# Performance work log

Hardware: AMD Instinct MI355X
Metric: run time of the kernel (lower is better)

## Reference

```python
import jax, jax.numpy as jnp
import numpy as np
from jax import lax

B, T, N, D, M, K, H = 16, 96, 256, 128, 1196, 8, 4
HD = D // H  # head dim = 32
TAU_TIME = 2.0


def setup_inputs() -> dict:
    key = jax.random.key(0)
    ks = jax.random.split(key, 12)
    w = lambda k, shp: jax.random.normal(k, shp, jnp.float32) * 0.05
    return {
        "x_scalar": jax.random.normal(ks[0], (B, T, N), jnp.float32),
        "season_q": jax.random.randint(ks[1], (B,), 0, 4),
        "year_q": 2010.0 + 10.0 * jax.random.uniform(ks[2], (B,), jnp.float32),
        "dw_w": w(ks[3], (N, 1, 12)),          # depthwise Conv1d weight (out=N, in/groups=1, k=12)
        "dw_b": jnp.zeros((N,), jnp.float32),
        "pw_w": w(ks[4], (N * D, N)),          # pointwise Conv1d weight (out=N*D, in=N), k=1 squeezed
        "pw_b": jnp.zeros((N * D,), jnp.float32),
        "ln_g": jnp.ones((D,), jnp.float32),
        "ln_b": jnp.zeros((D,), jnp.float32),
        "memory_bank": jax.random.normal(ks[5], (M, N, D), jnp.float32),
        "memory_seasons": jax.random.randint(ks[6], (M,), 0, 4),
        "memory_years": 2010.0 + 10.0 * jax.random.uniform(ks[7], (M,), jnp.float32),
        "in_proj_w": w(ks[8], (3 * D, D)),     # MHA packed q/k/v projection
        "in_proj_b": jnp.zeros((3 * D,), jnp.float32),
        "out_proj_w": w(ks[9], (D, D)),
        "out_proj_b": jnp.zeros((D,), jnp.float32),
        "proj_w": w(ks[10], (D, D)),
        "proj_b": jnp.zeros((D,), jnp.float32),
    }


def _layernorm(x, g, b, eps=1e-5):
    mu = jnp.mean(x, axis=-1, keepdims=True)
    var = jnp.mean((x - mu) ** 2, axis=-1, keepdims=True)
    return (x - mu) * lax.rsqrt(var + eps) * g + b


def _l2norm(x, eps=1e-12):
    n = jnp.sqrt(jnp.sum(x * x, axis=-1, keepdims=True))
    return x / jnp.maximum(n, eps)


def _forward(x_scalar, season_q, year_q, dw_w, dw_b, pw_w, pw_b, ln_g, ln_b,
             memory_bank, memory_seasons, memory_years,
             in_proj_w, in_proj_b, out_proj_w, out_proj_b, proj_w, proj_b):
    b, t, n = x_scalar.shape
    d = ln_g.shape[0]
    m = memory_bank.shape[0]

    # --- TemporalEncoder ---
    x = jnp.transpose(x_scalar, (0, 2, 1))  # (b, n, t): permute(0,2,3,1).reshape with d_input=1
    x = lax.conv_general_dilated(
        x, dw_w, window_strides=(1,), padding=[(6, 6)],
        dimension_numbers=("NCH", "OIH", "NCH"), feature_group_count=n)
    x = jax.nn.gelu(x + dw_b[:, None], approximate=False)      # (b, n, t+1)
    x = jnp.einsum("bct,oc->bot", x, pw_w) + pw_b[:, None]     # pointwise 1x1 conv -> (b, n*d, t+1)
    x = jax.nn.gelu(x, approximate=False)
    x = jnp.mean(x, axis=-1).reshape(b, n, d)                  # adaptive avg pool to 1
    q = _layernorm(x, ln_g, ln_b)                              # (b, n, d)

    # --- retrieve ---
    qf = _l2norm(q.reshape(b, n * d))
    memf = _l2norm(memory_bank.reshape(m, n * d))
    sim = qf @ memf.T                                          # (b, m)
    smask = (season_q[:, None] == memory_seasons[None, :]).astype(sim.dtype)
    sim = sim * smask + (1.0 - smask) * (-10000.0)
    dy = jnp.abs(year_q[:, None] - memory_years[None, :])
    diversity = 1.0 - jnp.exp(-dy / max(TAU_TIME, 1e-4))
    sim = sim * (0.5 + 0.5 * diversity)
    _, idx = lax.top_k(sim, K)                                 # (b, K)
    retrieved = memory_bank[idx]                               # (b, K, n, d)

    # --- cross attention: query (b*n, 1, d) vs kv (b*n, K, d) ---
    Wq, Wk, Wv = in_proj_w[:d], in_proj_w[d:2 * d], in_proj_w[2 * d:]
    bq, bk, bv = in_proj_b[:d], in_proj_b[d:2 * d], in_proj_b[2 * d:]
    kv = jnp.transpose(retrieved, (0, 2, 1, 3))                # (b, n, K, d)
    qp = (jnp.einsum("bnd,ed->bne", q, Wq) + bq).reshape(b, n, H, HD)
    kp = (jnp.einsum("bnkd,ed->bnke", kv, Wk) + bk).reshape(b, n, K, H, HD)
    vp = (jnp.einsum("bnkd,ed->bnke", kv, Wv) + bv).reshape(b, n, K, H, HD)
    scores = jnp.einsum("bnhe,bnkhe->bnhk", qp, kp) / np.sqrt(HD)
    attn = jax.nn.softmax(scores, axis=-1)
    ctx = jnp.einsum("bnhk,bnkhe->bnhe", attn, vp).reshape(b, n, d)
    out = jnp.einsum("bnd,ed->bne", ctx, out_proj_w) + out_proj_b
    out = jnp.einsum("bnd,ed->bne", out, proj_w) + proj_b
    return out, q


def reference(x_scalar, season_q, year_q, dw_w, dw_b, pw_w, pw_b, ln_g, ln_b,
              memory_bank, memory_seasons, memory_years,
              in_proj_w, in_proj_b, out_proj_w, out_proj_b, proj_w, proj_b):
    return _forward(x_scalar, season_q, year_q, dw_w, dw_b, pw_w, pw_b, ln_g, ln_b,
                    memory_bank, memory_seasons, memory_years,
                    in_proj_w, in_proj_b, out_proj_w, out_proj_b, proj_w, proj_b)
```

## Files before the change

kernel.cpp:

```cpp
#include <hip/hip_runtime.h>

typedef _Float16 f16x8 __attribute__((ext_vector_type(8)));
typedef _Float16 f16x4 __attribute__((ext_vector_type(4)));
typedef float    f32x4 __attribute__((ext_vector_type(4)));

__device__ __forceinline__ float gelu_f(float x) {
    float z  = 0.70710678118654752440f * x;
    float az = fabsf(z);
    float t  = 1.0f / fmaf(0.3275911f, az, 1.0f);
    float e  = __expf(-az * az);
    float p  = t * fmaf(t, fmaf(t, fmaf(t, fmaf(t, 1.061405429f, -1.453152027f),
                                        1.421413741f), -0.284496736f), 0.254829592f);
    float er = fmaf(-p, e, 1.0f);
    float s  = (z < 0.0f) ? -er : er;
    return 0.5f * x * (1.0f + s);
}

__device__ __forceinline__ void gload16(const void* g, void* l) {
    __builtin_amdgcn_global_load_lds(
        (const __attribute__((address_space(1))) unsigned int*)g,
        (__attribute__((address_space(3))) unsigned int*)l, 16, 0, 0);
}

__global__ void conv_kernel(const float* __restrict__ xs, const float* __restrict__ dww,
                            const float* __restrict__ dwb, _Float16* __restrict__ Gt)
{
    int b = blockIdx.x, t = blockIdx.y, n = threadIdx.x;
    float g = 0.f;
    if (t < 97) {
        float y = 0.f;
        #pragma unroll
        for (int j = 0; j < 12; ++j) {
            int tt = t + j - 6;
            if (tt >= 0 && tt < 96)
                y += dww[n*12 + j] * xs[((size_t)b*96 + tt)*256 + n];
        }
        g = gelu_f(y + dwb[n]);
    }
    Gt[((size_t)b*128 + t)*256 + n] = (_Float16)g;
}

__global__ void cvt_pw_kernel(const float* __restrict__ src, _Float16* __restrict__ dst,
                              const float* __restrict__ ipw, const float* __restrict__ opw,
                              const float* __restrict__ pjw, const float* __restrict__ opb,
                              const float* __restrict__ pjb, _Float16* __restrict__ wAll,
                              float* __restrict__ zp, _Float16* __restrict__ Wcf,
                              float* __restrict__ bc)
{
    int bid = blockIdx.x, tid = threadIdx.x;
    if (bid < 8192) {
        size_t i = ((size_t)bid*256 + tid) * 4;
        float4 v = *(const float4*)&src[i];
        f16x4 o; o[0] = (_Float16)v.x; o[1] = (_Float16)v.y; o[2] = (_Float16)v.z; o[3] = (_Float16)v.w;
        *(f16x4*)&dst[i] = o;
    } else if (bid < 8512) {
        int i = (bid - 8192)*256 + tid;
        float v = (i < 49152) ? ipw[i] : (i < 65536 ? opw[i - 49152] : pjw[i - 65536]);
        wAll[i] = (_Float16)v;
    } else if (bid < 8532) {
        int i = (bid - 8512)*256 + tid;
        if (i < 5087) {
            float4 z = {0.f, 0.f, 0.f, 0.f};
            *(float4*)&zp[i*4] = z;
        }
    } else {
        int e = (bid - 8532)*2 + (tid >> 7);
        int c = tid & 127;
        float acc = 0.f;
        for (int d = 0; d < 128; ++d)
            acc = fmaf(pjw[e*128 + d], opw[d*128 + c], acc);
        Wcf[e*128 + c] = (_Float16)acc;
        if (c == 0) {
            float s = pjb[e];
            for (int d = 0; d < 128; ++d)
                s = fmaf(pjw[e*128 + d], opb[d], s);
            bc[e] = s;
        }
    }
}

__global__ __launch_bounds__(256) void pw_kernel(const _Float16* __restrict__ W,
                                                 const _Float16* __restrict__ Gt,
                                                 const float* __restrict__ pwb,
                                                 const float* __restrict__ lng,
                                                 const float* __restrict__ lnb,
                                                 float* __restrict__ qout,
                                                 _Float16* __restrict__ qh,
                                                 _Float16* __restrict__ qlo,
                                                 float* __restrict__ qss)
{
    __shared__ __align__(16) _Float16 As[2][128][32];
    __shared__ __align__(16) _Float16 Bs[2][128][32];

    int x = blockIdx.x;
    int xcd = x & 7, ii = x >> 3;
    int ob = xcd * 32 + (ii >> 4);
    int b  = ii & 15;
    const _Float16* Arow = W  + (size_t)ob * 128 * 256;
    const _Float16* Brow = Gt + (size_t)b  * 128 * 256;

    int tid = threadIdx.x, w = tid >> 6, l = tid & 63, lr = l & 15, lk = l >> 4;
    int wr = w >> 1, wc = w & 1;
    int rsw = (lr >> 1) & 3;

    f32x4 acc[4][4];
    #pragma unroll
    for (int i = 0; i < 4; ++i)
        #pragma unroll
        for (int j = 0; j < 4; ++j)
            acc[i][j] = f32x4{0.f, 0.f, 0.f, 0.f};

    auto stage = [&](int buf, int k0) {
        #pragma unroll
        for (int j = 0; j < 2; ++j) {
            int chunk = tid + j*256;
            int row = chunk >> 2;
            int co  = (chunk & 3) * 8;
            int cos = ((chunk & 3) ^ ((chunk >> 3) & 3)) * 8;
            gload16(&Arow[row*256 + k0 + cos], &As[buf][row][co]);
            gload16(&Brow[row*256 + k0 + cos], &Bs[buf][row][co]);
        }
    };

    stage(0, 0);
    __syncthreads();
    for (int ks = 0; ks < 8; ++ks) {
        int cur = ks & 1;
        if (ks < 7) stage(cur ^ 1, (ks + 1) * 32);
        f16x8 a[4], bb[4];
        #pragma unroll
        for (int i = 0; i < 4; ++i)
            a[i]  = *(const f16x8*)&As[cur][wr*64 + i*16 + lr][(lk ^ rsw)*8];
        #pragma unroll
        for (int j = 0; j < 4; ++j)
            if (wc == 0 || j < 3)
                bb[j] = *(const f16x8*)&Bs[cur][wc*64 + j*16 + lr][(lk ^ rsw)*8];
        #pragma unroll
        for (int i = 0; i < 4; ++i)
            #pragma unroll
            for (int j = 0; j < 4; ++j)
                if (wc == 0 || j < 3)
                    acc[i][j] = __builtin_amdgcn_mfma_f32_16x16x32_f16(bb[j], a[i], acc[i][j], 0, 0, 0);
        __syncthreads();
    }

    float (*red)[2] = reinterpret_cast<float(*)[2]>(&As[0][0][0]);
    #pragma unroll
    for (int i = 0; i < 4; ++i) {
        int og = ob*128 + wr*64 + i*16 + lr;
        float pbv = pwb[og];
        float s = 0.f;
        if (wc == 0) {
            #pragma unroll
            for (int j = 0; j < 4; ++j)
                #pragma unroll
                for (int r = 0; r < 4; ++r)
                    s += gelu_f(acc[i][j][r] + pbv);
        } else {
            #pragma unroll
            for (int j = 0; j < 2; ++j)
                #pragma unroll
                for (int r = 0; r < 4; ++r)
                    s += gelu_f(acc[i][j][r] + pbv);
            if (lk == 0) s += gelu_f(acc[i][2][0] + pbv);
        }
        s += __shfl_xor(s, 16, 64);
        s += __shfl_xor(s, 32, 64);
        if (lk == 0) red[wr*64 + i*16 + lr][wc] = s;
    }
    __syncthreads();

    if (w == 0) {
        float x0 = (red[l][0]      + red[l][1])      * (1.f/97.f);
        float x1 = (red[64 + l][0] + red[64 + l][1]) * (1.f/97.f);
        float sm = x0 + x1;
        #pragma unroll
        for (int m = 1; m < 64; m <<= 1) sm += __shfl_xor(sm, m, 64);
        float mu = sm * (1.f/128.f);
        float d0 = x0 - mu, d1 = x1 - mu;
        float vv = d0*d0 + d1*d1;
        #pragma unroll
        for (int m = 1; m < 64; m <<= 1) vv += __shfl_xor(vv, m, 64);
        float rs = 1.0f / sqrtf(vv * (1.f/128.f) + 1e-5f);
        float q0 = d0*rs*lng[l]      + lnb[l];
        float q1 = d1*rs*lng[64 + l] + lnb[64 + l];
        size_t bn = (size_t)b*256 + ob;
        qout[bn*128 + l]      = q0;
        qout[bn*128 + 64 + l] = q1;
        _Float16 h0 = (_Float16)q0, h1 = (_Float16)q1;
        qh[bn*128 + l]       = h0;
        qh[bn*128 + 64 + l]  = h1;
        qlo[bn*128 + l]      = (_Float16)(q0 - (float)h0);
        qlo[bn*128 + 64 + l] = (_Float16)(q1 - (float)h1);
        float ss = q0*q0 + q1*q1;
        #pragma unroll
        for (int m = 1; m < 64; m <<= 1) ss += __shfl_xor(ss, m, 64);
        if (l == 0) atomicAdd(&qss[b], ss);
    }
}

__global__ __launch_bounds__(256) void simgemm_kernel(const _Float16* __restrict__ qhi,
                                                      const _Float16* __restrict__ qlo,
                                                      const float* __restrict__ mem,
                                                      float* __restrict__ dotp,
                                                      float* __restrict__ mn2)
{
    __shared__ __align__(16) float Ms[2][16][256];
    __shared__ f32x4 redls[4][64];
    __shared__ float redn[4][16];

    int tid = threadIdx.x, w = tid >> 6, l = tid & 63, lr = l & 15, lk = l >> 4;
    int m0 = blockIdx.y * 16;
    int kwin = blockIdx.x * 1024;
    int rowm = m0 + lr;

    auto stage = [&](int buf, int sw) {
        #pragma unroll
        for (int j = 0; j < 4; ++j) {
            int r = w*4 + j;
            int rowg = m0 + r; if (rowg > 1195) rowg = 1195;
            const float* src = mem + (size_t)rowg*32768 + kwin + sw*256 + (l ^ (r & 7))*4;
            gload16(src, &Ms[buf][r][0]);
        }
    };

    f32x4 acc_a = {0.f,0.f,0.f,0.f}, acc_b = {0.f,0.f,0.f,0.f};
    float nacc = 0.f;

    stage(0, 0);
    __syncthreads();
    for (int sw = 0; sw < 4; ++sw) {
        int cur = sw & 1;
        if (sw < 3) stage(cur ^ 1, sw + 1);
        #pragma unroll
        for (int cc = 0; cc < 2; ++cc) {
            int kl = w*64 + cc*32;
            int s0 = (kl + lk*8) >> 2;
            float4 v0 = *(const float4*)&Ms[cur][lr][(s0       ^ (lr & 7))*4];
            float4 v1 = *(const float4*)&Ms[cur][lr][((s0 + 1) ^ (lr & 7))*4];
            int kg = kwin + sw*256 + kl + lk*8;
            f16x8 ah = *(const f16x8*)&qhi[(size_t)lr*32768 + kg];
            f16x8 al = *(const f16x8*)&qlo[(size_t)lr*32768 + kg];
            float e0 = v0.x, e1 = v0.y, e2 = v0.z, e3 = v0.w;
            float e4 = v1.x, e5 = v1.y, e6 = v1.z, e7 = v1.w;
            f16x8 bh;
            bh[0]=(_Float16)e0; bh[1]=(_Float16)e1; bh[2]=(_Float16)e2; bh[3]=(_Float16)e3;
            bh[4]=(_Float16)e4; bh[5]=(_Float16)e5; bh[6]=(_Float16)e6; bh[7]=(_Float16)e7;
            nacc = fmaf(e0,e0, fmaf(e1,e1, fmaf(e2,e2, fmaf(e3,e3, nacc))));
            nacc = fmaf(e4,e4, fmaf(e5,e5, fmaf(e6,e6, fmaf(e7,e7, nacc))));
            acc_a = __builtin_amdgcn_mfma_f32_16x16x32_f16(ah, bh, acc_a, 0, 0, 0);
            acc_b = __builtin_amdgcn_mfma_f32_16x16x32_f16(al, bh, acc_b, 0, 0, 0);
        }
        __syncthreads();
    }

    nacc += __shfl_xor(nacc, 16, 64);
    nacc += __shfl_xor(nacc, 32, 64);

    f32x4 tot = acc_a + acc_b;
    redls[w][l] = tot;
    if (lk == 0) redn[w][lr] = nacc;
    __syncthreads();
    if (w == 0) {
        tot = redls[0][l];
        tot += redls[1][l]; tot += redls[2][l]; tot += redls[3][l];
        if (rowm < 1196) {
            #pragma unroll
            for (int r = 0; r < 4; ++r)
                atomicAdd(&dotp[(lk*4 + r)*1196 + rowm], tot[r]);
            if (lk == 0)
                atomicAdd(&mn2[rowm], redn[0][lr] + redn[1][lr] + redn[2][lr] + redn[3][lr]);
        }
    }
}

__global__ void topk_kernel(const float* __restrict__ dotp, const float* __restrict__ mn2,
                            const float* __restrict__ qss, const int* __restrict__ seaq,
                            const float* __restrict__ yq, const int* __restrict__ seam,
                            const float* __restrict__ ym, int* __restrict__ idx)
{
    __shared__ float sc[1216];
    int b = blockIdx.x, lane = threadIdx.x;
    float qn = fmaxf(sqrtf(qss[b]), 1e-12f);
    int sq = seaq[b];
    float yqv = yq[b];
    for (int m = lane; m < 1216; m += 64) {
        float v = -3e38f;
        if (m < 1196) {
            float s = dotp[b*1196 + m] / (qn * fmaxf(sqrtf(mn2[m]), 1e-12f));
            if (seam[m] != sq) s = -10000.0f;
            float dy = fabsf(yqv - ym[m]);
            v = s * (1.0f - 0.5f * expf(-0.5f * dy));
        }
        sc[m] = v;
    }
    __syncthreads();
    for (int kk = 0; kk < 8; ++kk) {
        float bv = -3e38f; int bi = 0x7fffffff;
        for (int m = lane; m < 1216; m += 64) {
            float v = sc[m];
            if (v > bv) { bv = v; bi = m; }
        }
        #pragma unroll
        for (int mk = 1; mk < 64; mk <<= 1) {
            float ov = __shfl_xor(bv, mk, 64);
            int   oi = __shfl_xor(bi, mk, 64);
            if (ov > bv || (ov == bv && oi < bi)) { bv = ov; bi = oi; }
        }
        if (lane == 0) { idx[b*8 + kk] = bi; sc[bi] = -3e38f; }
        __syncthreads();
    }
}

__global__ __launch_bounds__(256) void qkv_kernel(const _Float16* __restrict__ qh,
                                                  const float* __restrict__ memb,
                                                  const int* __restrict__ idx,
                                                  const _Float16* __restrict__ wAll,
                                                  const float* __restrict__ ipb,
                                                  _Float16* __restrict__ qp,
                                                  _Float16* __restrict__ kp,
                                                  _Float16* __restrict__ vp)
{
    int bid = blockIdx.x;
    const _Float16* Wm; const float* bias; _Float16* Y; int blk; int kv;
    if (bid < 64)       { kv = 0; Wm = wAll;         bias = ipb;       Y = qp; blk = bid; }
    else if (bid < 576) { kv = 1; Wm = wAll + 16384; bias = ipb + 128; Y = kp; blk = bid - 64; }
    else                { kv = 1; Wm = wAll + 32768; bias = ipb + 256; Y = vp; blk = bid - 576; }

    int tid = threadIdx.x, w = tid >> 6, l = tid & 63, lr = l & 15, lk = l >> 4;
    int r0 = blk * 64 + w * 16;

    const float* Af = nullptr;
    const _Float16* Ah = nullptr;
    if (kv) {
        int bk = (blk * 64) >> 8;
        int row = idx[bk];
        Af = memb + (size_t)row*32768 + ((r0 & 255) + lr)*128 + lk*8;
    } else {
        Ah = qh + (size_t)(r0 + lr)*128 + lk*8;
    }

    f32x4 acc[8];
    #pragma unroll
    for (int j = 0; j < 8; ++j) acc[j] = f32x4{0.f, 0.f, 0.f, 0.f};
    #pragma unroll
    for (int k0 = 0; k0 < 128; k0 += 32) {
        f16x8 a;
        if (kv) {
            float4 v0 = *(const float4*)&Af[k0];
            float4 v1 = *(const float4*)&Af[k0 + 4];
            a[0]=(_Float16)v0.x; a[1]=(_Float16)v0.y; a[2]=(_Float16)v0.z; a[3]=(_Float16)v0.w;
            a[4]=(_Float16)v1.x; a[5]=(_Float16)v1.y; a[6]=(_Float16)v1.z; a[7]=(_Float16)v1.w;
        } else {
            a = *(const f16x8*)&Ah[k0];
        }
        #pragma unroll
        for (int j = 0; j < 8; ++j) {
            f16x8 bb = *(const f16x8*)&Wm[(j*16 + lr)*128 + k0 + lk*8];
            acc[j] = __builtin_amdgcn_mfma_f32_16x16x32_f16(a, bb, acc[j], 0, 0, 0);
        }
    }
    #pragma unroll
    for (int j = 0; j < 8; ++j) {
        #pragma unroll
        for (int r = 0; r < 4; ++r) {
            int row = r0 + lk*4 + r, col = j*16 + lr;
            Y[(size_t)row*128 + col] = (_Float16)(acc[j][r] + bias[col]);
        }
    }
}

__global__ void attn_kernel(const _Float16* __restrict__ qp, const _Float16* __restrict__ kp,
                            const _Float16* __restrict__ vp, const _Float16* __restrict__ Wc,
                            const float* __restrict__ bc, float* __restrict__ outp)
{
    __shared__ float ctxs[128];
    int bn = blockIdx.x;
    int b = bn >> 8, n = bn & 255;
    int tid = threadIdx.x;
    float qv = (float)qp[(size_t)bn*128 + tid];
    float sc[8];
    #pragma unroll
    for (int k = 0; k < 8; ++k) {
        float p = qv * (float)kp[(((size_t)(b*8 + k)*256 + n)*128) + tid];
        #pragma unroll
        for (int m = 1; m < 32; m <<= 1) p += __shfl_xor(p, m, 64);
        sc[k] = p * 0.17677669529663687f;
    }
    float mx = sc[0];
    #pragma unroll
    for (int k = 1; k < 8; ++k) mx = fmaxf(mx, sc[k]);
    float den = 0.f;
    #pragma unroll
    for (int k = 0; k < 8; ++k) { sc[k] = expf(sc[k] - mx); den += sc[k]; }
    float inv = 1.f / den;
    float c = 0.f;
    #pragma unroll
    for (int k = 0; k < 8; ++k)
        c += sc[k] * (float)vp[(((size_t)(b*8 + k)*256 + n)*128) + tid];
    ctxs[tid] = c * inv;
    __syncthreads();

    float s = bc[tid];
    const f16x8* wrow = (const f16x8*)&Wc[(size_t)tid*128];
    #pragma unroll
    for (int c0 = 0; c0 < 16; ++c0) {
        f16x8 wv = wrow[c0];
        #pragma unroll
        for (int u = 0; u < 8; ++u)
            s = fmaf(ctxs[c0*8 + u], (float)wv[u], s);
    }
    outp[(size_t)bn*128 + tid] = s;
}

extern "C" void kernel_launch(void* const* d_in, const int* in_sizes, int n_in,
                              void* d_out, int out_size, void* d_ws, size_t ws_size,
                              hipStream_t stream)
{
    const float* x_scalar = (const float*)d_in[0];
    const int*   season_q = (const int*)d_in[1];
    const float* year_q   = (const float*)d_in[2];
    const float* dw_w     = (const float*)d_in[3];
    const float* dw_b     = (const float*)d_in[4];
    const float* pw_w     = (const float*)d_in[5];
    const float* pw_b     = (const float*)d_in[6];
    const float* ln_g     = (const float*)d_in[7];
    const float* ln_b     = (const float*)d_in[8];
    const float* memb     = (const float*)d_in[9];
    const int*   mseas    = (const int*)d_in[10];
    const float* myear    = (const float*)d_in[11];
    const float* ipw      = (const float*)d_in[12];
    const float* ipb      = (const float*)d_in[13];
    const float* opw      = (const float*)d_in[14];
    const float* opb      = (const float*)d_in[15];
    const float* pjw      = (const float*)d_in[16];
    const float* pjb      = (const float*)d_in[17];

    char* wsb = (char*)d_ws;
    _Float16* Wf   = (_Float16*)(wsb + 0);
    _Float16* Gt   = (_Float16*)(wsb + 16777216);
    float*    qss  = (float*)   (wsb + 20971520);
    float*    dotp = (float*)   (wsb + 20971584);
    float*    mn2  = (float*)   (wsb + 21048128);
    int*      idxb = (int*)     (wsb + 21052928);
    _Float16* qp   = (_Float16*)(wsb + 29442048);
    _Float16* kp   = (_Float16*)(wsb + 30490624);
    _Float16* vp   = (_Float16*)(wsb + 38879232);
    _Float16* Wcf  = (_Float16*)(wsb + 48316416);
    float*    bc   = (float*)   (wsb + 48349184);
    _Float16* wAll = (_Float16*)(wsb + 49364992);
    _Float16* qlo  = (_Float16*)(wsb + 49528832);
    _Float16* qh   = (_Float16*)(wsb + 19922944);

    float* outp = (float*)d_out;
    float* qout = (float*)d_out + 524288;

    cvt_pw_kernel<<<8596, 256, 0, stream>>>(pw_w, Wf, ipw, opw, pjw, opb, pjb, wAll,
                                            (float*)(wsb + 20971520), Wcf, bc);
    conv_kernel<<<dim3(16, 128), 256, 0, stream>>>(x_scalar, dw_w, dw_b, Gt);

    pw_kernel<<<4096, 256, 0, stream>>>(Wf, Gt, pw_b, ln_g, ln_b, qout, qh, qlo, qss);

    simgemm_kernel<<<dim3(32, 75), 256, 0, stream>>>(qh, qlo, memb, dotp, mn2);
    topk_kernel<<<16, 64, 0, stream>>>(dotp, mn2, qss, season_q, year_q, mseas, myear, idxb);

    qkv_kernel<<<1088, 256, 0, stream>>>(qh, memb, idxb, wAll, ipb, qp, kp, vp);

    attn_kernel<<<4096, 128, 0, stream>>>(qp, kp, vp, Wcf, bc, outp);
}
```

Before: 203.6 us.

## Tile-transpose query halves for simgemm loads and fuse K/V projections

```diff
diff --git a/kernel.cpp b/kernel.cpp
--- a/kernel.cpp
+++ b/kernel.cpp
@@ -86,7 +86,8 @@
                                                  const float* __restrict__ lnb,
                                                  float* __restrict__ qout,
                                                  _Float16* __restrict__ qh,
-                                                 _Float16* __restrict__ qlo,
+                                                 _Float16* __restrict__ qhT,
+                                                 _Float16* __restrict__ qloT,
                                                  float* __restrict__ qss)
 {
     __shared__ __align__(16) _Float16 As[2][128][32];
@@ -190,8 +191,12 @@
         _Float16 h0 = (_Float16)q0, h1 = (_Float16)q1;
         qh[bn*128 + l]       = h0;
         qh[bn*128 + 64 + l]  = h1;
-        qlo[bn*128 + l]      = (_Float16)(q0 - (float)h0);
-        qlo[bn*128 + 64 + l] = (_Float16)(q1 - (float)h1);
+        int ch0 = ob*4 + (l >> 5);
+        int sub = b*32 + ((l >> 3) & 3)*8 + (l & 7);
+        qhT [ch0*512 + sub]       = h0;
+        qhT [(ch0 + 2)*512 + sub] = h1;
+        qloT[ch0*512 + sub]       = (_Float16)(q0 - (float)h0);
+        qloT[(ch0 + 2)*512 + sub] = (_Float16)(q1 - (float)h1);
         float ss = q0*q0 + q1*q1;
         #pragma unroll
         for (int m = 1; m < 64; m <<= 1) ss += __shfl_xor(ss, m, 64);
@@ -199,8 +204,8 @@
     }
 }
 
-__global__ __launch_bounds__(256) void simgemm_kernel(const _Float16* __restrict__ qhi,
-                                                      const _Float16* __restrict__ qlo,
+__global__ __launch_bounds__(256) void simgemm_kernel(const _Float16* __restrict__ qhT,
+                                                      const _Float16* __restrict__ qloT,
                                                       const float* __restrict__ mem,
                                                       float* __restrict__ dotp,
                                                       float* __restrict__ mn2)
@@ -238,9 +243,10 @@
             int s0 = (kl + lk*8) >> 2;
             float4 v0 = *(const float4*)&Ms[cur][lr][(s0       ^ (lr & 7))*4];
             float4 v1 = *(const float4*)&Ms[cur][lr][((s0 + 1) ^ (lr & 7))*4];
-            int kg = kwin + sw*256 + kl + lk*8;
-            f16x8 ah = *(const f16x8*)&qhi[(size_t)lr*32768 + kg];
-            f16x8 al = *(const f16x8*)&qlo[(size_t)lr*32768 + kg];
+            int chunk = (kwin + sw*256 + kl) >> 5;
+            int fo = lr*4 + lk;
+            f16x8 ah = ((const f16x8*)(qhT  + (size_t)chunk*512))[fo];
+            f16x8 al = ((const f16x8*)(qloT + (size_t)chunk*512))[fo];
             float e0 = v0.x, e1 = v0.y, e2 = v0.z, e3 = v0.w;
             float e4 = v1.x, e5 = v1.y, e6 = v1.z, e7 = v1.w;
             f16x8 bh;
@@ -322,50 +328,66 @@
                                                   _Float16* __restrict__ vp)
 {
     int bid = blockIdx.x;
-    const _Float16* Wm; const float* bias; _Float16* Y; int blk; int kv;
-    if (bid < 64)       { kv = 0; Wm = wAll;         bias = ipb;       Y = qp; blk = bid; }
-    else if (bid < 576) { kv = 1; Wm = wAll + 16384; bias = ipb + 128; Y = kp; blk = bid - 64; }
-    else                { kv = 1; Wm = wAll + 32768; bias = ipb + 256; Y = vp; blk = bid - 576; }
-
     int tid = threadIdx.x, w = tid >> 6, l = tid & 63, lr = l & 15, lk = l >> 4;
-    int r0 = blk * 64 + w * 16;
-
-    const float* Af = nullptr;
-    const _Float16* Ah = nullptr;
-    if (kv) {
+
+    if (bid < 64) {
+        int r0 = bid * 64 + w * 16;
+        const _Float16* Ah = qh + (size_t)(r0 + lr)*128 + lk*8;
+        f32x4 acc[8];
+        #pragma unroll
+        for (int j = 0; j < 8; ++j) acc[j] = f32x4{0.f, 0.f, 0.f, 0.f};
+        #pragma unroll
+        for (int k0 = 0; k0 < 128; k0 += 32) {
+            f16x8 a = *(const f16x8*)&Ah[k0];
+            #pragma unroll
+            for (int j = 0; j < 8; ++j) {
+                f16x8 bb = *(const f16x8*)&wAll[(j*16 + lr)*128 + k0 + lk*8];
+                acc[j] = __builtin_amdgcn_mfma_f32_16x16x32_f16(a, bb, acc[j], 0, 0, 0);
+            }
+        }
+        #pragma unroll
+        for (int j = 0; j < 8; ++j) {
+            #pragma unroll
+            for (int r = 0; r < 4; ++r) {
+                int row = r0 + lk*4 + r, col = j*16 + lr;
+                qp[(size_t)row*128 + col] = (_Float16)(acc[j][r] + ipb[col]);
+            }
+        }
+    } else {
+        int blk = bid - 64;
+        int r0 = blk * 64 + w * 16;
         int bk = (blk * 64) >> 8;
         int row = idx[bk];
-        Af = memb + (size_t)row*32768 + ((r0 & 255) + lr)*128 + lk*8;
-    } else {
-        Ah = qh + (size_t)(r0 + lr)*128 + lk*8;
-    }
-
-    f32x4 acc[8];
-    #pragma unroll
-    for (int j = 0; j < 8; ++j) acc[j] = f32x4{0.f, 0.f, 0.f, 0.f};
-    #pragma unroll
-    for (int k0 = 0; k0 < 128; k0 += 32) {
-        f16x8 a;
-        if (kv) {
+        const float* Af = memb + (size_t)row*32768 + ((r0 & 255) + lr)*128 + lk*8;
+        const _Float16* Wk = wAll + 16384;
+        const _Float16* Wv = wAll + 32768;
+
+        f32x4 acck[8], accv[8];
+        #pragma unroll
+        for (int j = 0; j < 8; ++j) { acck[j] = f32x4{0.f,0.f,0.f,0.f}; accv[j] = f32x4{0.f,0.f,0.f,0.f}; }
+        #pragma unroll
+        for (int k0 = 0; k0 < 128; k0 += 32) {
             float4 v0 = *(const float4*)&Af[k0];
             float4 v1 = *(const float4*)&Af[k0 + 4];
+            f16x8 a;
             a[0]=(_Float16)v0.x; a[1]=(_Float16)v0.y; a[2]=(_Float16)v0.z; a[3]=(_Float16)v0.w;
             a[4]=(_Float16)v1.x; a[5]=(_Float16)v1.y; a[6]=(_Float16)v1.z; a[7]=(_Float16)v1.w;
-        } else {
-            a = *(const f16x8*)&Ah[k0];
+            #pragma unroll
+            for (int j = 0; j < 8; ++j) {
+                f16x8 bk_ = *(const f16x8*)&Wk[(j*16 + lr)*128 + k0 + lk*8];
+                acck[j] = __builtin_amdgcn_mfma_f32_16x16x32_f16(a, bk_, acck[j], 0, 0, 0);
+                f16x8 bv_ = *(const f16x8*)&Wv[(j*16 + lr)*128 + k0 + lk*8];
+                accv[j] = __builtin_amdgcn_mfma_f32_16x16x32_f16(a, bv_, accv[j], 0, 0, 0);
+            }
         }
         #pragma unroll
         for (int j = 0; j < 8; ++j) {
-            f16x8 bb = *(const f16x8*)&Wm[(j*16 + lr)*128 + k0 + lk*8];
-            acc[j] = __builtin_amdgcn_mfma_f32_16x16x32_f16(a, bb, acc[j], 0, 0, 0);
-        }
-    }
-    #pragma unroll
-    for (int j = 0; j < 8; ++j) {
-        #pragma unroll
-        for (int r = 0; r < 4; ++r) {
-            int row = r0 + lk*4 + r, col = j*16 + lr;
-            Y[(size_t)row*128 + col] = (_Float16)(acc[j][r] + bias[col]);
+            #pragma unroll
+            for (int r = 0; r < 4; ++r) {
+                int row2 = r0 + lk*4 + r, col = j*16 + lr;
+                kp[(size_t)row2*128 + col] = (_Float16)(acck[j][r] + ipb[128 + col]);
+                vp[(size_t)row2*128 + col] = (_Float16)(accv[j][r] + ipb[256 + col]);
+            }
         }
     }
 }
@@ -439,6 +461,8 @@
     char* wsb = (char*)d_ws;
     _Float16* Wf   = (_Float16*)(wsb + 0);
     _Float16* Gt   = (_Float16*)(wsb + 16777216);
+    _Float16* qloT = (_Float16*)(wsb + 17825792);
+    _Float16* qh   = (_Float16*)(wsb + 19922944);
     float*    qss  = (float*)   (wsb + 20971520);
     float*    dotp = (float*)   (wsb + 20971584);
     float*    mn2  = (float*)   (wsb + 21048128);
@@ -449,8 +473,7 @@
     _Float16* Wcf  = (_Float16*)(wsb + 48316416);
     float*    bc   = (float*)   (wsb + 48349184);
     _Float16* wAll = (_Float16*)(wsb + 49364992);
-    _Float16* qlo  = (_Float16*)(wsb + 49528832);
-    _Float16* qh   = (_Float16*)(wsb + 19922944);
+    _Float16* qhT  = (_Float16*)(wsb + 49528832);
 
     float* outp = (float*)d_out;
     float* qout = (float*)d_out + 524288;
@@ -459,12 +482,12 @@
                                             (float*)(wsb + 20971520), Wcf, bc);
     conv_kernel<<<dim3(16, 128), 256, 0, stream>>>(x_scalar, dw_w, dw_b, Gt);
 
-    pw_kernel<<<4096, 256, 0, stream>>>(Wf, Gt, pw_b, ln_g, ln_b, qout, qh, qlo, qss);
-
-    simgemm_kernel<<<dim3(32, 75), 256, 0, stream>>>(qh, qlo, memb, dotp, mn2);
+    pw_kernel<<<4096, 256, 0, stream>>>(Wf, Gt, pw_b, ln_g, ln_b, qout, qh, qhT, qloT, qss);
+
+    simgemm_kernel<<<dim3(32, 75), 256, 0, stream>>>(qhT, qloT, memb, dotp, mn2);
     topk_kernel<<<16, 64, 0, stream>>>(dotp, mn2, qss, season_q, year_q, mseas, myear, idxb);
 
-    qkv_kernel<<<1088, 256, 0, stream>>>(qh, memb, idxb, wAll, ipb, qp, kp, vp);
+    qkv_kernel<<<576, 256, 0, stream>>>(qh, memb, idxb, wAll, ipb, qp, kp, vp);
 
     attn_kernel<<<4096, 128, 0, stream>>>(qp, kp, vp, Wcf, bc, outp);
 }
```

Result: faster. 198.9 us (median of 3 runs) (-2.3%).
